# Performance work log

Measured on AMD Instinct MI355X. Metric: run time of the kernel, lower is better.

Reference implementation:

```python
import jax, jax.numpy as jnp
import numpy as np

B, S, L, D = 16, 1024, 512, 1024
H = 8
DH = D // H
WD = 256          # word/type embedding dim
VOCAB = 1000      # type vocab
NEG = -1e30


def setup_inputs() -> dict:
    key = jax.random.key(0)
    ks = jax.random.split(key, 16)
    inv = 1.0 / np.sqrt(D)
    return {
        "encoder_outs": jax.random.normal(ks[0], (B, S, D), dtype=jnp.float32),
        "to_sem": jax.random.randint(ks[1], (B, L), 0, S, dtype=jnp.int64),
        "to_sem_type": jax.random.randint(ks[2], (B, L), 0, VOCAB, dtype=jnp.int64),
        "sem_syn": jax.random.randint(ks[3], (B, S), 0, L + 1, dtype=jnp.int64),
        "wq": jax.random.normal(ks[4], (D, D), dtype=jnp.float32) * inv,
        "bq": jnp.zeros((D,), dtype=jnp.float32),
        "wk": jax.random.normal(ks[5], (D, D), dtype=jnp.float32) * inv,
        "bk": jnp.zeros((D,), dtype=jnp.float32),
        "wv": jax.random.normal(ks[6], (D, D), dtype=jnp.float32) * inv,
        "bv": jnp.zeros((D,), dtype=jnp.float32),
        "wo": jax.random.normal(ks[7], (D, D), dtype=jnp.float32) * inv,
        "bo": jnp.zeros((D,), dtype=jnp.float32),
        "type_emb": jax.random.normal(ks[8], (VOCAB, WD), dtype=jnp.float32),
        "w_proj": jax.random.normal(ks[9], (D, D + WD), dtype=jnp.float32) / np.sqrt(D + WD),
        "b_proj": jnp.zeros((D,), dtype=jnp.float32),
        "bias_root": jax.random.normal(ks[10], (1, 1, D), dtype=jnp.float32),
    }


def _forward(encoder_outs, to_sem, to_sem_type, sem_syn,
             wq, bq, wk, bk, wv, bv, wo, bo,
             type_emb, w_proj, b_proj, bias_root):
    bsz, len_sem = to_sem.shape
    src_len = encoder_outs.shape[1]

    # batch_index_select: gather the encoder states at semantic head positions
    sem_vec = jnp.take_along_axis(encoder_outs, to_sem[:, :, None], axis=1)  # [B,L,D]

    # Vectorized mask build (replaces the Python loop + scatter):
    # buf[b,i,j] = (sem_syn[b,j] == i+1) or (j == to_sem[b,i])
    ids = jnp.arange(1, len_sem + 1, dtype=sem_syn.dtype)
    aligned = sem_syn[:, None, :] == ids[None, :, None]                       # [B,L,S]
    self_pos = jnp.arange(src_len)[None, None, :] == to_sem[:, :, None]       # [B,L,S]
    allow = aligned | self_pos                                                # [B,L,S]

    # fairseq-style MHA: q scaled by head_dim**-0.5, in/out proj with bias
    q = (sem_vec @ wq.T + bq) * (DH ** -0.5)
    k = encoder_outs @ wk.T + bk
    v = encoder_outs @ wv.T + bv
    q = q.reshape(bsz, len_sem, H, DH)
    k = k.reshape(bsz, src_len, H, DH)
    v = v.reshape(bsz, src_len, H, DH)

    scores = jnp.einsum("blhd,bshd->bhls", q, k)                              # [B,H,L,S]
    scores = jnp.where(allow[:, None, :, :], scores, NEG)
    attn = jax.nn.softmax(scores, axis=-1)
    ctx = jnp.einsum("bhls,bshd->blhd", attn, v).reshape(bsz, len_sem, D)
    sem_vec = ctx @ wo.T + bo                                                 # [B,L,D]

    # arg/type embedding + concat + projection
    type_vec = type_emb[to_sem_type]                                          # [B,L,WD]
    embedding = jnp.concatenate([sem_vec, type_vec], axis=-1) @ w_proj.T + b_proj

    root = jnp.broadcast_to(bias_root, (bsz, 1, D))
    return embedding, jnp.concatenate([root, embedding], axis=1)


def reference(encoder_outs, to_sem, to_sem_type, sem_syn,
              wq, bq, wk, bk, wv, bv, wo, bo,
              type_emb, w_proj, b_proj, bias_root):
    return _forward(encoder_outs, to_sem, to_sem_type, sem_syn,
                    wq, bq, wk, bk, wv, bv, wo, bo,
                    type_emb, w_proj, b_proj, bias_root)
```

## Files before the change

### kernel.cpp

```cpp
#include <hip/hip_runtime.h>

typedef unsigned short u16;
typedef unsigned int   u32;
typedef unsigned long long u64;
typedef __bf16 bf16x8 __attribute__((ext_vector_type(8)));
typedef float  f32x4  __attribute__((ext_vector_type(4)));

#define B_  16
#define S_  1024
#define L_  512
#define D_  1024
#define H_  8
#define WD_ 256
#define KP_ (D_ + WD_)

__device__ __forceinline__ u16 f2bf(float f) {
    u32 u = __float_as_uint(f);
    return (u16)((u + 0x7FFFu + ((u >> 16) & 1u)) >> 16);
}
__device__ __forceinline__ float bf2f(u16 h) {
    return __uint_as_float(((u32)h) << 16);
}
__device__ __forceinline__ void gload16(const void* g, void* l) {
    __builtin_amdgcn_global_load_lds(
        (const __attribute__((address_space(1))) u32*)(unsigned long long)(g),
        (__attribute__((address_space(3))) u32*)(unsigned long long)(l),
        16, 0, 0);
}

__global__ __launch_bounds__(256) void prep_k(
    const float* __restrict__ enc,
    const float* __restrict__ wk, const float* __restrict__ wv,
    const float* __restrict__ wq, const float* __restrict__ te,
    const float* __restrict__ bk, const float* __restrict__ bv,
    const float* __restrict__ bq,
    const float* __restrict__ wo, const float* __restrict__ wproj,
    const float* __restrict__ bo, const float* __restrict__ bproj,
    u16* __restrict__ enc_bf, u16* __restrict__ wkvq, u16* __restrict__ te_bf,
    float* __restrict__ bkvq, u16* __restrict__ wot,
    u16* __restrict__ wp1, u16* __restrict__ wfin,
    float* __restrict__ beff, float qs)
{
    __shared__ float tile[64][65];
    const int bid = blockIdx.x;
    if (bid < 16384) {
        const int i = (bid * 256 + threadIdx.x) * 4;
        const float4 v = *(const float4*)(enc + i);
        ushort4 o;
        o.x = f2bf(v.x); o.y = f2bf(v.y); o.z = f2bf(v.z); o.w = f2bf(v.w);
        *(ushort4*)(enc_bf + i) = o;
    } else if (bid < 19456) {
        const int b2 = bid - 16384;
        const int plane = b2 >> 10;
        const int i = ((b2 & 1023) * 256 + threadIdx.x) * 4;
        const float* src = plane == 0 ? wk : (plane == 1 ? wv : wq);
        const float s = plane == 2 ? qs : 1.0f;
        const float4 v = *(const float4*)(src + i);
        ushort4 o;
        o.x = f2bf(v.x * s); o.y = f2bf(v.y * s); o.z = f2bf(v.z * s); o.w = f2bf(v.w * s);
        *(ushort4*)(wkvq + (size_t)plane * 1048576 + i) = o;
    } else if (bid < 19706) {
        const int i = ((bid - 19456) * 256 + threadIdx.x) * 4;
        if (i < 256000) {
            const float4 v = *(const float4*)(te + i);
            ushort4 o;
            o.x = f2bf(v.x); o.y = f2bf(v.y); o.z = f2bf(v.z); o.w = f2bf(v.w);
            *(ushort4*)(te_bf + i) = o;
        }
    } else if (bid < 19709) {
        const int i = (bid - 19706) * 1024 + threadIdx.x * 4;
        #pragma unroll
        for (int j = 0; j < 4; ++j) {
            const int idx = i + j;
            bkvq[idx] = (idx < 1024) ? bk[idx]
                      : (idx < 2048 ? bv[idx - 1024] : bq[idx - 2048] * qs);
        }
    } else if (bid < 19965) {
        const int cid = bid - 19709;
        const int t0 = (cid & 15) * 64;
        const int k0 = (cid >> 4) * 64;
        const int tr = threadIdx.x >> 4;
        const int tc = threadIdx.x & 15;
        #pragma unroll
        for (int i = 0; i < 4; ++i) {
            const int r = tr + i * 16;
            const float4 v = *(const float4*)(wo + (size_t)(t0 + r) * 1024 + k0 + tc * 4);
            tile[r][tc * 4 + 0] = v.x; tile[r][tc * 4 + 1] = v.y;
            tile[r][tc * 4 + 2] = v.z; tile[r][tc * 4 + 3] = v.w;
        }
        __syncthreads();
        #pragma unroll
        for (int i = 0; i < 4; ++i) {
            const int r = tr + i * 16;
            ushort4 o;
            o.x = f2bf(tile[tc * 4 + 0][r]);
            o.y = f2bf(tile[tc * 4 + 1][r]);
            o.z = f2bf(tile[tc * 4 + 2][r]);
            o.w = f2bf(tile[tc * 4 + 3][r]);
            *(ushort4*)(wot + (size_t)(k0 + r) * 1024 + t0 + tc * 4) = o;
        }
    } else if (bid < 21245) {
        const int i = ((bid - 19965) * 256 + threadIdx.x) * 4;
        const int n = i / 1280, c = i % 1280;
        const float4 v = *(const float4*)(wproj + i);
        ushort4 o;
        o.x = f2bf(v.x); o.y = f2bf(v.y); o.z = f2bf(v.z); o.w = f2bf(v.w);
        if (c < 1024) *(ushort4*)(wp1 + (size_t)n * 1024 + c) = o;
        else          *(ushort4*)(wfin + (size_t)n * 1280 + c) = o;
    } else {
        const int w = threadIdx.x >> 6, lane = threadIdx.x & 63;
        const int n = (bid - 21245) * 4 + w;
        const float* row = wproj + (size_t)n * 1280;
        float s = 0.f;
        for (int t = lane; t < 1024; t += 64) s += row[t] * bo[t];
        #pragma unroll
        for (int off = 32; off > 0; off >>= 1) s += __shfl_down(s, off);
        if (lane == 0) beff[n] = bproj[n] + s;
    }
}

template <int NT>
__global__ __launch_bounds__(1024, 4) void mm8_k(
    const u16* __restrict__ A, const u16* __restrict__ W,
    const float* __restrict__ bias,
    u16* __restrict__ o0, u16* __restrict__ o1,
    int K, int ntn)
{
    __shared__ alignas(16) u16 lds[65536];
    const int tid  = threadIdx.x;
    const int w    = tid >> 6;
    const int lane = tid & 63;
    const int l15  = lane & 15;
    const int lk   = lane >> 4;
    const int wr   = w >> 2;
    const int wc   = w & 3;

    const int nwg = gridDim.x;
    const int bid = blockIdx.x;
    const int e   = (bid & 7) * (nwg >> 3) + (bid >> 3);
    const int bm0 = (e / ntn) * 256;
    const int bn0 = (e % ntn) * 256;

    const int kc_l = (lane & 3) ^ ((lane >> 3) & 3);
    const u16* gsrc = (w < 8) ? A : W;
    const int rbase = (w < 8) ? bm0 : bn0;
    size_t src[2];
    #pragma unroll
    for (int i = 0; i < 2; ++i) {
        const int row = (w & 7) * 32 + i * 16 + (lane >> 2);
        src[i] = (size_t)(rbase + row) * K + kc_l * 8;
    }
    const int dstA = ((w < 8) ? 0 : 8192) + (w & 7) * 1024;

#define STAGE(t) { u16* d = lds + ((t) & 3) * 16384 + dstA;            \
    gload16(gsrc + src[0] + (size_t)(t) * 32, d);                      \
    gload16(gsrc + src[1] + (size_t)(t) * 32, d + 512); }

    const int rslot = (lk ^ ((l15 >> 1) & 3)) * 8;
    const int aoff = (wr * 64 + l15) * 32 + rslot;
    const int boff = 8192 + (wc * 64 + l15) * 32 + rslot;

    f32x4 acc[4][4] = {};

    STAGE(0); STAGE(1); STAGE(2);
    asm volatile("s_waitcnt vmcnt(4)" ::: "memory");
    __builtin_amdgcn_sched_barrier(0);
    __builtin_amdgcn_s_barrier();

    for (int t = 0; t < NT; ++t) {
        const u16* sa = lds + (t & 3) * 16384 + aoff;
        const u16* sb = lds + (t & 3) * 16384 + boff;
        bf16x8 af[4], bfr[4];
        #pragma unroll
        for (int nf = 0; nf < 4; ++nf) bfr[nf] = *(const bf16x8*)(sb + nf * 512);
        #pragma unroll
        for (int mf = 0; mf < 4; ++mf) af[mf] = *(const bf16x8*)(sa + mf * 512);
        if (t + 3 < NT) STAGE(t + 3);
        __builtin_amdgcn_s_setprio(1);
        #pragma unroll
        for (int mf = 0; mf < 4; ++mf)
            #pragma unroll
            for (int nf = 0; nf < 4; ++nf)
                acc[mf][nf] = __builtin_amdgcn_mfma_f32_16x16x32_bf16(af[mf], bfr[nf], acc[mf][nf], 0, 0, 0);
        __builtin_amdgcn_s_setprio(0);
        if (t < NT - 3)      { asm volatile("s_waitcnt vmcnt(4)" ::: "memory"); }
        else if (t == NT - 3){ asm volatile("s_waitcnt vmcnt(2)" ::: "memory"); }
        else if (t == NT - 2){ asm volatile("s_waitcnt vmcnt(0)" ::: "memory"); }
        __builtin_amdgcn_sched_barrier(0);
        __builtin_amdgcn_s_barrier();
    }
#undef STAGE

    const int plane = bn0 >> 10;
    u16* outp = plane == 0 ? o0 : o1;
    const int cip0 = (bn0 & 1023) + wc * 64;
    const int colg = bn0 + wc * 64 + l15;
    float bsv[4];
    #pragma unroll
    for (int nf = 0; nf < 4; ++nf) bsv[nf] = bias[colg + nf * 16];
    const int erow = lane >> 3;
    const int echk = lane & 7;
    u16* wlds = lds + w * 2304;

    #pragma unroll
    for (int mf = 0; mf < 4; ++mf) {
        u16* pat = wlds + (mf & 1) * 1152;
        #pragma unroll
        for (int nf = 0; nf < 4; ++nf) {
            #pragma unroll
            for (int r = 0; r < 4; ++r) {
                const float val = acc[mf][nf][r] + bsv[nf];
                const float pv = __shfl_xor(val, 1, 64);
                if ((l15 & 1) == 0) {
                    const u32 pk = (u32)f2bf(val) | ((u32)f2bf(pv) << 16);
                    *(u32*)(pat + (lk * 4 + r) * 72 + nf * 16 + l15) = pk;
                }
            }
        }
        asm volatile("s_waitcnt lgkmcnt(0)" ::: "memory");
        __builtin_amdgcn_sched_barrier(0);
        #pragma unroll
        for (int j2 = 0; j2 < 2; ++j2) {
            const int rr = j2 * 8 + erow;
            const uint4 vv = *(const uint4*)(pat + rr * 72 + echk * 8);
            const int grow = bm0 + wr * 64 + mf * 16 + rr;
            *(uint4*)(outp + (size_t)grow * 1024 + cip0 + echk * 8) = vv;
        }
    }
}

__global__ __launch_bounds__(256) void qw_k(
    const u16* __restrict__ enc_bf, const u16* __restrict__ wq_w,
    const float* __restrict__ bq_s, u16* __restrict__ q_out,
    const u16* __restrict__ wp1, const u16* __restrict__ wot,
    u16* __restrict__ wfin, const int* __restrict__ to_sem)
{
    __shared__ alignas(16) u16 lds[32768];

    const int bid  = blockIdx.x;
    const bool isQ = bid < 512;
    const int tid  = threadIdx.x;
    const int wid  = tid >> 6;
    const int lane = tid & 63;
    const int l15  = lane & 15;
    const int lk   = lane >> 4;

    const u16* pA; const u16* pW; const float* pB; u16* pO; int ostride; int e;
    if (isQ) {
        e = (bid & 7) * 64 + (bid >> 3);
        pA = enc_bf; pW = wq_w; pB = bq_s; pO = q_out; ostride = 1024;
    } else {
        const int b2 = bid - 512;
        e = (b2 & 7) * 8 + (b2 >> 3);
        pA = wp1; pW = wot; pB = nullptr; pO = wfin; ostride = 1280;
    }
    const int bm0 = (e >> 3) * 128;
    const int bn0 = (e & 7) * 128;

    const int kc_l = (lane & 3) ^ ((lane >> 3) & 3);
    long ga[2], gw[2];
    #pragma unroll
    for (int i = 0; i < 2; ++i) {
        const int row = wid * 32 + i * 16 + (lane >> 2);
        const int m = bm0 + row;
        ga[i] = isQ ? ((long)(m >> 9) * S_ + to_sem[m]) * D_ + kc_l * 8
                    : (long)m * 1024 + kc_l * 8;
        gw[i] = (long)(bn0 + row) * 1024 + kc_l * 8;
    }

#define QSTAGE(t) { const int k0t = (t) * 32;                              \
    u16* d  = lds + ((t) & 3) * 8192 + wid * 1024;                         \
    u16* db = d + 4096;                                                    \
    gload16(pA + ga[0] + k0t, d);                                          \
    gload16(pA + ga[1] + k0t, d + 512);                                    \
    gload16(pW + gw[0] + k0t, db);                                         \
    gload16(pW + gw[1] + k0t, db + 512); }

    f32x4 acc[4][4] = {};

    const int moff = (wid >> 1) * 64;
    const int noff = (wid & 1) * 64;
    const int rslot = (lk ^ ((l15 >> 1) & 3)) * 8;
    const int aoff = (moff + l15) * 32 + rslot;
    const int boff = 4096 + (noff + l15) * 32 + rslot;

    QSTAGE(0); QSTAGE(1); QSTAGE(2);
    asm volatile("s_waitcnt vmcnt(8)" ::: "memory");
    __builtin_amdgcn_sched_barrier(0);
    __builtin_amdgcn_s_barrier();

    for (int t = 0; t < 32; ++t) {
        const u16* sa = lds + (t & 3) * 8192 + aoff;
        const u16* sb = lds + (t & 3) * 8192 + boff;
        bf16x8 af[4], bfr[4];
        #pragma unroll
        for (int j = 0; j < 4; ++j) bfr[j] = *(const bf16x8*)(sb + j * 512);
        #pragma unroll
        for (int i = 0; i < 4; ++i) af[i] = *(const bf16x8*)(sa + i * 512);
        if (t + 3 < 32) QSTAGE(t + 3);
        __builtin_amdgcn_s_setprio(1);
        #pragma unroll
        for (int i = 0; i < 4; ++i)
            #pragma unroll
            for (int j = 0; j < 4; ++j)
                acc[i][j] = __builtin_amdgcn_mfma_f32_16x16x32_bf16(af[i], bfr[j], acc[i][j], 0, 0, 0);
        __builtin_amdgcn_s_setprio(0);
        if (t < 29)      { asm volatile("s_waitcnt vmcnt(8)" ::: "memory"); }
        else if (t == 29){ asm volatile("s_waitcnt vmcnt(4)" ::: "memory"); }
        else if (t == 30){ asm volatile("s_waitcnt vmcnt(0)" ::: "memory"); }
        __builtin_amdgcn_sched_barrier(0);
        __builtin_amdgcn_s_barrier();
    }
#undef QSTAGE

    #pragma unroll
    for (int j = 0; j < 4; ++j) {
        const int col = bn0 + noff + j * 16 + l15;
        const float bj = pB ? pB[col] : 0.f;
        #pragma unroll
        for (int i = 0; i < 4; ++i) {
            const int mrow = bm0 + moff + i * 16 + lk * 4;
            #pragma unroll
            for (int r = 0; r < 4; ++r)
                pO[(long)(mrow + r) * ostride + col] = f2bf(acc[i][j][r] + bj);
        }
    }
}

__global__ __launch_bounds__(256) void fin_k(
    const u16* __restrict__ A, const u16* __restrict__ W,
    const float* __restrict__ bias,
    float* __restrict__ Yf, float* __restrict__ Y2,
    const int* __restrict__ gidx, const u16* __restrict__ aux,
    const float* __restrict__ broot)
{
    constexpr int NT = 40;
    __shared__ alignas(16) u16 lds[32768];

    const int bid = blockIdx.x;
    if (bid >= 512) {
        const int i = (bid - 512) * 256 + threadIdx.x;
        const int b = i >> 10, d = i & 1023;
        Y2[(size_t)b * (L_ + 1) * D_ + d] = broot[d];
        return;
    }

    const int tid  = threadIdx.x;
    const int wid  = tid >> 6;
    const int lane = tid & 63;
    const int l15  = lane & 15;
    const int lk   = lane >> 4;

    const int e   = (bid & 7) * 64 + (bid >> 3);
    const int bm0 = (e >> 3) * 128;
    const int bn0 = (e & 7) * 128;

    const int kc_l = (lane & 3) ^ ((lane >> 3) & 3);
    long ga[2], gw[2], gt[2];
    #pragma unroll
    for (int i = 0; i < 2; ++i) {
        const int row = wid * 32 + i * 16 + (lane >> 2);
        const int m = bm0 + row;
        ga[i] = (long)m * D_ + kc_l * 8;
        gt[i] = (long)gidx[m] * WD_ + kc_l * 8;
        gw[i] = (long)(bn0 + row) * KP_ + kc_l * 8;
    }

#define FSTAGE(t) { const int k0t = (t) * 32;                              \
    u16* d  = lds + ((t) & 3) * 8192 + wid * 1024;                         \
    u16* db = d + 4096;                                                    \
    if (k0t >= D_) {                                                       \
        gload16(aux + gt[0] + (k0t - D_), d);                              \
        gload16(aux + gt[1] + (k0t - D_), d + 512);                        \
    } else {                                                               \
        gload16(A + ga[0] + k0t, d);                                       \
        gload16(A + ga[1] + k0t, d + 512);                                 \
    }                                                                      \
    gload16(W + gw[0] + k0t, db);                                          \
    gload16(W + gw[1] + k0t, db + 512); }

    f32x4 acc[4][4] = {};

    const int moff = (wid >> 1) * 64;
    const int noff = (wid & 1) * 64;
    const int rslot = (lk ^ ((l15 >> 1) & 3)) * 8;
    const int aoff = (moff + l15) * 32 + rslot;
    const int boff = 4096 + (noff + l15) * 32 + rslot;

    FSTAGE(0); FSTAGE(1); FSTAGE(2);
    asm volatile("s_waitcnt vmcnt(8)" ::: "memory");
    __builtin_amdgcn_sched_barrier(0);
    __builtin_amdgcn_s_barrier();

    for (int t = 0; t < NT; ++t) {
        const u16* sa = lds + (t & 3) * 8192 + aoff;
        const u16* sb = lds + (t & 3) * 8192 + boff;
        bf16x8 af[4], bfr[4];
        #pragma unroll
        for (int j = 0; j < 4; ++j) bfr[j] = *(const bf16x8*)(sb + j * 512);
        #pragma unroll
        for (int i = 0; i < 4; ++i) af[i] = *(const bf16x8*)(sa + i * 512);
        if (t + 3 < NT) FSTAGE(t + 3);
        __builtin_amdgcn_s_setprio(1);
        #pragma unroll
        for (int i = 0; i < 4; ++i)
            #pragma unroll
            for (int j = 0; j < 4; ++j)
                acc[i][j] = __builtin_amdgcn_mfma_f32_16x16x32_bf16(af[i], bfr[j], acc[i][j], 0, 0, 0);
        __builtin_amdgcn_s_setprio(0);
        if (t < NT - 3)      { asm volatile("s_waitcnt vmcnt(8)" ::: "memory"); }
        else if (t == NT - 3){ asm volatile("s_waitcnt vmcnt(4)" ::: "memory"); }
        else if (t == NT - 2){ asm volatile("s_waitcnt vmcnt(0)" ::: "memory"); }
        __builtin_amdgcn_sched_barrier(0);
        __builtin_amdgcn_s_barrier();
    }
#undef FSTAGE

    #pragma unroll
    for (int j = 0; j < 4; ++j) {
        const int col = bn0 + noff + j * 16 + l15;
        const float bj = bias[col];
        #pragma unroll
        for (int i = 0; i < 4; ++i) {
            const int mrow = bm0 + moff + i * 16 + lk * 4;
            #pragma unroll
            for (int r = 0; r < 4; ++r) {
                const float val = acc[i][j][r] + bj;
                const long m = mrow + r;
                Yf[m * (long)D_ + col] = val;
                const long bb = m >> 9, ll = m & 511;
                Y2[((bb * (L_ + 1)) + ll + 1) * (long)D_ + col] = val;
            }
        }
    }
}

__global__ __launch_bounds__(256) void attn_k(
    const u16* __restrict__ kb, const u16* __restrict__ vb,
    const int* __restrict__ sem_syn, const int* __restrict__ to_sem,
    const u16* __restrict__ qf, u16* __restrict__ ctx)
{
    __shared__ int   list[S_];
    __shared__ float sc[H_][S_];
    __shared__ int   wcnt[16];

    const int bl  = blockIdx.x;
    const int b   = bl >> 9;
    const int l   = bl & 511;
    const int tid = threadIdx.x;
    const int wvi = tid >> 6;
    const int ln  = tid & 63;

    const int tosem = to_sem[bl];
    const ushort4 qu = *(const ushort4*)(qf + (size_t)bl * D_ + tid * 4);
    const float4 qv = make_float4(bf2f(qu.x), bf2f(qu.y), bf2f(qu.z), bf2f(qu.w));

    bool al[4];
    #pragma unroll
    for (int j = 0; j < 4; ++j) {
        const int s = tid * 4 + j;
        const int a = sem_syn[b * S_ + s];
        al[j] = (a == l + 1) || (s == tosem);
    }
    u64 msk[4];
    #pragma unroll
    for (int j = 0; j < 4; ++j) msk[j] = __ballot(al[j]);
    if (ln == 0) {
        #pragma unroll
        for (int j = 0; j < 4; ++j) wcnt[wvi * 4 + j] = __popcll(msk[j]);
    }
    __syncthreads();
    int mybase[4];
    {
        int tot = 0;
        #pragma unroll
        for (int i2 = 0; i2 < 16; ++i2) {
            const int c2 = wcnt[i2];
            #pragma unroll
            for (int j2 = 0; j2 < 4; ++j2)
                if (i2 == wvi * 4 + j2) mybase[j2] = tot;
            tot += c2;
        }
    }
    const u64 lmlt = (1ull << ln) - 1ull;
    #pragma unroll
    for (int j = 0; j < 4; ++j)
        if (al[j]) list[mybase[j] + __popcll(msk[j] & lmlt)] = tid * 4 + j;
    int n = 0;
    #pragma unroll
    for (int i2 = 0; i2 < 16; ++i2) n += wcnt[i2];
    __syncthreads();

    const int g = tid >> 5;
    const int lane = tid & 31;
    for (int i = 0; i < n; ++i) {
        const u16* krow = kb + ((size_t)b * S_ + list[i]) * D_;
        const ushort4 ku = *(const ushort4*)(krow + tid * 4);
        float p = bf2f(ku.x) * qv.x + bf2f(ku.y) * qv.y + bf2f(ku.z) * qv.z + bf2f(ku.w) * qv.w;
        #pragma unroll
        for (int off = 16; off > 0; off >>= 1) p += __shfl_down(p, off, 32);
        if (lane == 0) sc[g][i] = p;
    }
    __syncthreads();

    float mx = -3.0e38f;
    for (int i = lane; i < n; i += 32) mx = fmaxf(mx, sc[g][i]);
    #pragma unroll
    for (int off = 16; off > 0; off >>= 1) mx = fmaxf(mx, __shfl_xor(mx, off, 32));
    float sum = 0.f;
    for (int i = lane; i < n; i += 32) {
        const float e = expf(sc[g][i] - mx);
        sc[g][i] = e;
        sum += e;
    }
    #pragma unroll
    for (int off = 16; off > 0; off >>= 1) sum += __shfl_xor(sum, off, 32);
    const float inv = 1.0f / sum;
    __syncthreads();

    float4 a4 = make_float4(0.f, 0.f, 0.f, 0.f);
    for (int i = 0; i < n; ++i) {
        const float wgt = sc[g][i] * inv;
        const u16* vrow = vb + ((size_t)b * S_ + list[i]) * D_;
        const ushort4 vu = *(const ushort4*)(vrow + tid * 4);
        a4.x = fmaf(wgt, bf2f(vu.x), a4.x);
        a4.y = fmaf(wgt, bf2f(vu.y), a4.y);
        a4.z = fmaf(wgt, bf2f(vu.z), a4.z);
        a4.w = fmaf(wgt, bf2f(vu.w), a4.w);
    }
    ushort4 o;
    o.x = f2bf(a4.x); o.y = f2bf(a4.y); o.z = f2bf(a4.z); o.w = f2bf(a4.w);
    *(ushort4*)(ctx + (size_t)bl * D_ + tid * 4) = o;
}

extern "C" void kernel_launch(void* const* d_in, const int* in_sizes, int n_in,
                              void* d_out, int out_size, void* d_ws, size_t ws_size,
                              hipStream_t stream)
{
    const float* enc    = (const float*)d_in[0];
    const int*   to_sem = (const int*)  d_in[1];
    const int*   tstype = (const int*)  d_in[2];
    const int*   semsyn = (const int*)  d_in[3];
    const float* wq = (const float*)d_in[4];
    const float* bq = (const float*)d_in[5];
    const float* wk = (const float*)d_in[6];
    const float* bk = (const float*)d_in[7];
    const float* wv = (const float*)d_in[8];
    const float* bv = (const float*)d_in[9];
    const float* wo = (const float*)d_in[10];
    const float* bo = (const float*)d_in[11];
    const float* temb  = (const float*)d_in[12];
    const float* wproj = (const float*)d_in[13];
    const float* bproj = (const float*)d_in[14];
    const float* broot = (const float*)d_in[15];

    float* out1 = (float*)d_out;
    float* out2 = out1 + (size_t)B_ * L_ * D_;

    unsigned char* ws = (unsigned char*)d_ws;
    u16*   enc_bf = (u16*)(ws);
    u16*   k_bf   = (u16*)(ws + (32ull << 20));
    u16*   wkvq   = (u16*)(ws + (64ull << 20));
    u16*   wot    = (u16*)(ws + (70ull << 20));
    u16*   wp1    = (u16*)(ws + (72ull << 20));
    u16*   wfin   = (u16*)(ws + (74ull << 20));
    float* beff   = (float*)(ws + (77ull << 20));
    float* bkvq   = (float*)(ws + (77ull << 20) + 8192);
    u16*   ctx_bf = (u16*)(ws + (78ull << 20));
    u16*   te_bf  = (u16*)(ws + (94ull << 20));

    u16* v_bf = (u16*)d_out;
    u16* q_bf = (u16*)((unsigned char*)d_out + (32ull << 20));

    const float qscale = 0.08838834764831845f;
    dim3 blk(256);

    prep_k<<<dim3(21501), blk, 0, stream>>>(
        enc, wk, wv, wq, temb, bk, bv, bq, wo, wproj, bo, bproj,
        enc_bf, wkvq, te_bf, bkvq, wot, wp1, wfin, beff, qscale);

    mm8_k<32><<<dim3(512), dim3(1024), 0, stream>>>(
        enc_bf, wkvq, bkvq, k_bf, v_bf, 1024, 8);

    qw_k<<<dim3(576), blk, 0, stream>>>(
        enc_bf, wkvq + 2097152, bkvq + 2048, q_bf, wp1, wot, wfin, to_sem);

    attn_k<<<dim3(B_ * L_), blk, 0, stream>>>(k_bf, v_bf, semsyn, to_sem, q_bf, ctx_bf);

    fin_k<<<dim3(576), blk, 0, stream>>>(
        ctx_bf, wfin, beff, out1, out2, tstype, te_bf, broot);
}
```

Baseline: 211.8 us.

## Rework K/V GEMM to 8-wave blocks with 128-row warp tiles and K=64 double buffering

New measurement: 214.8 us. Within noise of the previous version (+1.4%).

```diff
diff --git a/kernel.cpp b/kernel.cpp
--- a/kernel.cpp
+++ b/kernel.cpp
@@ -120,7 +120,7 @@
 }
 
 template <int NT>
-__global__ __launch_bounds__(1024, 4) void mm8_k(
+__global__ __launch_bounds__(512, 2) void mm64_k(
     const u16* __restrict__ A, const u16* __restrict__ W,
     const float* __restrict__ bias,
     u16* __restrict__ o0, u16* __restrict__ o1,
@@ -142,40 +142,42 @@
     const int bn0 = (e % ntn) * 256;
 
     const int kc_l = (lane & 3) ^ ((lane >> 3) & 3);
-    const u16* gsrc = (w < 8) ? A : W;
-    const int rbase = (w < 8) ? bm0 : bn0;
-    size_t src[2];
+    size_t asrc[2], bsrc[2];
     #pragma unroll
     for (int i = 0; i < 2; ++i) {
-        const int row = (w & 7) * 32 + i * 16 + (lane >> 2);
-        src[i] = (size_t)(rbase + row) * K + kc_l * 8;
-    }
-    const int dstA = ((w < 8) ? 0 : 8192) + (w & 7) * 1024;
-
-#define STAGE(t) { u16* d = lds + ((t) & 3) * 16384 + dstA;            \
-    gload16(gsrc + src[0] + (size_t)(t) * 32, d);                      \
-    gload16(gsrc + src[1] + (size_t)(t) * 32, d + 512); }
+        const int row = w * 32 + i * 16 + (lane >> 2);
+        asrc[i] = (size_t)(bm0 + row) * K + kc_l * 8;
+        bsrc[i] = (size_t)(bn0 + row) * K + kc_l * 8;
+    }
+    const int dst = w * 1024;
+
+#define STG_A(t, kh) { u16* d = lds + ((t) & 1) * 32768 + (kh) * 16384 + dst;      \
+    gload16(A + asrc[0] + (size_t)(t) * 64 + (kh) * 32, d);                        \
+    gload16(A + asrc[1] + (size_t)(t) * 64 + (kh) * 32, d + 512); }
+#define STG_B(t, kh) { u16* d = lds + ((t) & 1) * 32768 + (kh) * 16384 + 8192 + dst; \
+    gload16(W + bsrc[0] + (size_t)(t) * 64 + (kh) * 32, d);                        \
+    gload16(W + bsrc[1] + (size_t)(t) * 64 + (kh) * 32, d + 512); }
 
     const int rslot = (lk ^ ((l15 >> 1) & 3)) * 8;
-    const int aoff = (wr * 64 + l15) * 32 + rslot;
+    const int aoff = (wr * 128 + l15) * 32 + rslot;
     const int boff = 8192 + (wc * 64 + l15) * 32 + rslot;
 
-    f32x4 acc[4][4] = {};
-
-    STAGE(0); STAGE(1); STAGE(2);
+    f32x4 acc[8][4] = {};
+
+    STG_A(0, 0); STG_B(0, 0); STG_A(0, 1); STG_B(0, 1);
     asm volatile("s_waitcnt vmcnt(4)" ::: "memory");
     __builtin_amdgcn_sched_barrier(0);
     __builtin_amdgcn_s_barrier();
 
     for (int t = 0; t < NT; ++t) {
-        const u16* sa = lds + (t & 3) * 16384 + aoff;
-        const u16* sb = lds + (t & 3) * 16384 + boff;
+        const u16* base = lds + (t & 1) * 32768;
         bf16x8 af[4], bfr[4];
         #pragma unroll
-        for (int nf = 0; nf < 4; ++nf) bfr[nf] = *(const bf16x8*)(sb + nf * 512);
-        #pragma unroll
-        for (int mf = 0; mf < 4; ++mf) af[mf] = *(const bf16x8*)(sa + mf * 512);
-        if (t + 3 < NT) STAGE(t + 3);
+        for (int nf = 0; nf < 4; ++nf) bfr[nf] = *(const bf16x8*)(base + boff + nf * 512);
+        #pragma unroll
+        for (int mf = 0; mf < 4; ++mf) af[mf] = *(const bf16x8*)(base + aoff + mf * 512);
+        if (t + 1 < NT) STG_A(t + 1, 0);
+        __builtin_amdgcn_s_barrier();
         __builtin_amdgcn_s_setprio(1);
         #pragma unroll
         for (int mf = 0; mf < 4; ++mf)
@@ -183,13 +185,55 @@
             for (int nf = 0; nf < 4; ++nf)
                 acc[mf][nf] = __builtin_amdgcn_mfma_f32_16x16x32_bf16(af[mf], bfr[nf], acc[mf][nf], 0, 0, 0);
         __builtin_amdgcn_s_setprio(0);
-        if (t < NT - 3)      { asm volatile("s_waitcnt vmcnt(4)" ::: "memory"); }
-        else if (t == NT - 3){ asm volatile("s_waitcnt vmcnt(2)" ::: "memory"); }
-        else if (t == NT - 2){ asm volatile("s_waitcnt vmcnt(0)" ::: "memory"); }
+        __builtin_amdgcn_s_barrier();
+        #pragma unroll
+        for (int mf = 0; mf < 4; ++mf) af[mf] = *(const bf16x8*)(base + aoff + (mf + 4) * 512);
+        if (t + 1 < NT) STG_B(t + 1, 0);
+        __builtin_amdgcn_s_barrier();
+        __builtin_amdgcn_s_setprio(1);
+        #pragma unroll
+        for (int mf = 0; mf < 4; ++mf)
+            #pragma unroll
+            for (int nf = 0; nf < 4; ++nf)
+                acc[mf + 4][nf] = __builtin_amdgcn_mfma_f32_16x16x32_bf16(af[mf], bfr[nf], acc[mf + 4][nf], 0, 0, 0);
+        __builtin_amdgcn_s_setprio(0);
+        if (t + 1 < NT) { asm volatile("s_waitcnt vmcnt(4)" ::: "memory"); }
+        else            { asm volatile("s_waitcnt vmcnt(0)" ::: "memory"); }
         __builtin_amdgcn_sched_barrier(0);
         __builtin_amdgcn_s_barrier();
-    }
-#undef STAGE
+        #pragma unroll
+        for (int nf = 0; nf < 4; ++nf) bfr[nf] = *(const bf16x8*)(base + 16384 + boff + nf * 512);
+        #pragma unroll
+        for (int mf = 0; mf < 4; ++mf) af[mf] = *(const bf16x8*)(base + 16384 + aoff + mf * 512);
+        if (t + 1 < NT) STG_A(t + 1, 1);
+        __builtin_amdgcn_s_barrier();
+        __builtin_amdgcn_s_setprio(1);
+        #pragma unroll
+        for (int mf = 0; mf < 4; ++mf)
+            #pragma unroll
+            for (int nf = 0; nf < 4; ++nf)
+                acc[mf][nf] = __builtin_amdgcn_mfma_f32_16x16x32_bf16(af[mf], bfr[nf], acc[mf][nf], 0, 0, 0);
+        __builtin_amdgcn_s_setprio(0);
+        __builtin_amdgcn_s_barrier();
+        #pragma unroll
+        for (int mf = 0; mf < 4; ++mf) af[mf] = *(const bf16x8*)(base + 16384 + aoff + (mf + 4) * 512);
+        if (t + 1 < NT) STG_B(t + 1, 1);
+        __builtin_amdgcn_s_barrier();
+        __builtin_amdgcn_s_setprio(1);
+        #pragma unroll
+        for (int mf = 0; mf < 4; ++mf)
+            #pragma unroll
+            for (int nf = 0; nf < 4; ++nf)
+                acc[mf + 4][nf] = __builtin_amdgcn_mfma_f32_16x16x32_bf16(af[mf], bfr[nf], acc[mf + 4][nf], 0, 0, 0);
+        __builtin_amdgcn_s_setprio(0);
+        if (t + 1 < NT) {
+            asm volatile("s_waitcnt vmcnt(4)" ::: "memory");
+            __builtin_amdgcn_sched_barrier(0);
+        }
+        __builtin_amdgcn_s_barrier();
+    }
+#undef STG_A
+#undef STG_B
 
     const int plane = bn0 >> 10;
     u16* outp = plane == 0 ? o0 : o1;
@@ -203,7 +247,7 @@
     u16* wlds = lds + w * 2304;
 
     #pragma unroll
-    for (int mf = 0; mf < 4; ++mf) {
+    for (int mf = 0; mf < 8; ++mf) {
         u16* pat = wlds + (mf & 1) * 1152;
         #pragma unroll
         for (int nf = 0; nf < 4; ++nf) {
@@ -223,7 +267,7 @@
         for (int j2 = 0; j2 < 2; ++j2) {
             const int rr = j2 * 8 + erow;
             const uint4 vv = *(const uint4*)(pat + rr * 72 + echk * 8);
-            const int grow = bm0 + wr * 64 + mf * 16 + rr;
+            const int grow = bm0 + wr * 128 + mf * 16 + rr;
             *(uint4*)(outp + (size_t)grow * 1024 + cip0 + echk * 8) = vv;
         }
     }
@@ -579,7 +623,7 @@
         enc, wk, wv, wq, temb, bk, bv, bq, wo, wproj, bo, bproj,
         enc_bf, wkvq, te_bf, bkvq, wot, wp1, wfin, beff, qscale);
 
-    mm8_k<32><<<dim3(512), dim3(1024), 0, stream>>>(
+    mm64_k<16><<<dim3(512), dim3(512), 0, stream>>>(
         enc_bf, wkvq, bkvq, k_bf, v_bf, 1024, 8);
 
     qw_k<<<dim3(576), blk, 0, stream>>>(
```
